# Kernel tuning notes

Measured on AMD Instinct MI355X. Metric: run time of the kernel, lower is better.

Reference implementation:

```python
import jax, jax.numpy as jnp
import numpy as np

B, T, H = 2, 2048, 2048
QH, KH, D = 16, 8, 128
F = 8192
EPS = 1e-06
MASK_VALUE = -1e30


def _rms_norm(x, gamma, eps=EPS):
    rms = jnp.sqrt(jnp.mean(x.astype(jnp.float32) ** 2, axis=-1, keepdims=True) + eps)
    return (gamma * x / rms).astype(jnp.bfloat16)


def _rope(x, sin, cos):
    # x: [B,T,h,D]; sin/cos: [B,T,D//2]
    x1, x2 = x[..., : x.shape[-1] // 2], x[..., x.shape[-1] // 2:]
    s, c = sin[:, :, None, :], cos[:, :, None, :]
    return jnp.concatenate([x1 * c - x2 * s, x2 * c + x1 * s], axis=-1)


def _attention(q, k, v, q_idx, k_idx, q_pos, k_pos):
    # q: [B,QH,T,D]; k,v: [B,KH,T,D]. Online-softmax tiling in the original is
    # mathematically identical to a single stable softmax over the full causal row.
    orig = q.dtype
    q = q.astype(jnp.float32)
    k = k.astype(jnp.float32)
    v = v.astype(jnp.float32)
    rep = q.shape[1] // k.shape[1]
    k = jnp.repeat(k, rep, axis=1)
    v = jnp.repeat(v, rep, axis=1)
    scale = 1.0 / jnp.sqrt(jnp.asarray(q.shape[-1], jnp.float32))
    s = jnp.einsum('bhqd,bhkd->bhqk', q, k) * scale
    mask = (q_idx[:, None, :, None] & k_idx[:, None, None, :]) & (
        q_pos[:, None, :, None] >= k_pos[:, None, None, :])
    s = jnp.where(mask, s, MASK_VALUE)
    p = jax.nn.softmax(s, axis=-1)
    o = jnp.einsum('bhqk,bhkd->bhqd', p, v)
    return o.astype(orig)


def _block(x, sin, cos, token_mask, pre_gamma, wq, wk, wv, q_gamma, k_gamma, wo,
           post_gamma, wg, wu, wd):
    bf = jnp.bfloat16
    Bx, Tx = x.shape[0], x.shape[1]
    x_norm = _rms_norm(x, pre_gamma)                     # bf16
    q = (x_norm @ wq.astype(bf)).reshape(Bx, Tx, QH, D)
    k = (x_norm @ wk.astype(bf)).reshape(Bx, Tx, KH, D)
    v = (x_norm @ wv.astype(bf)).reshape(Bx, Tx, KH, D)
    q = _rope(_rms_norm(q, q_gamma), sin, cos)           # promotes to f32 (matches flax)
    k = _rope(_rms_norm(k, k_gamma), sin, cos)
    idx = token_mask != 0
    pos = jax.lax.broadcasted_iota(jnp.int32, token_mask.shape, 1)
    attn = _attention(q.swapaxes(1, 2), k.swapaxes(1, 2), v.swapaxes(1, 2),
                      idx, idx, pos, pos)
    attn = attn.swapaxes(1, 2).reshape(Bx, Tx, QH * D)
    x = x + attn.astype(bf) @ wo.astype(bf)
    x_norm = _rms_norm(x, post_gamma)
    g = jax.nn.silu(x_norm @ wg.astype(bf))
    y = g * (x_norm @ wu.astype(bf))
    x = x + y @ wd.astype(bf)
    return x, k, v


def setup_inputs() -> dict:
    key = jax.random.key(0)
    ks = jax.random.split(key, 8)

    def w(kk, shape):
        return jax.random.normal(kk, shape, jnp.float32) * 0.02

    x = jax.random.normal(ks[0], (B, T, H), jnp.float32)
    pos = jnp.arange(T, dtype=jnp.float32)
    inv_freq = 1.0 / (10000.0 ** (jnp.arange(D // 2, dtype=jnp.float32) / (D // 2)))
    ang = pos[:, None] * inv_freq[None, :]
    sin = jnp.broadcast_to(jnp.sin(ang)[None], (B, T, D // 2))
    cos = jnp.broadcast_to(jnp.cos(ang)[None], (B, T, D // 2))
    return {
        'x': x, 'sin': sin, 'cos': cos,
        'token_mask': jnp.ones((B, T), jnp.int32),
        'layer_id': 0,
        'pre_gamma': jnp.ones((H,), jnp.float32),
        'wq': w(ks[1], (H, QH * D)),
        'wk': w(ks[2], (H, KH * D)),
        'wv': w(ks[3], (H, KH * D)),
        'q_gamma': jnp.ones((D,), jnp.float32),
        'k_gamma': jnp.ones((D,), jnp.float32),
        'wo': w(ks[4], (QH * D, H)),
        'post_gamma': jnp.ones((H,), jnp.float32),
        'wg': w(ks[5], (H, F)),
        'wu': w(ks[6], (H, F)),
        'wd': w(ks[7], (F, H)),
    }


def reference(x, sin, cos, token_mask, layer_id, pre_gamma, wq, wk, wv, q_gamma,
              k_gamma, wo, post_gamma, wg, wu, wd):
    # cache=None path: layer_id is unused.
    return _block(x, sin, cos, token_mask, pre_gamma, wq, wk, wv, q_gamma,
                  k_gamma, wo, post_gamma, wg, wu, wd)
```

## Files before the change

kernel.cpp:

```cpp
#include <hip/hip_runtime.h>
#include <hip/hip_bf16.h>


#define Bc  2
#define Tc  2048
#define Hc  2048
#define QHc 16
#define KHc 8
#define Dc  128
#define Fc  8192
#define Mc  (Bc*Tc)
#define FCHUNK 2048
#define EPSc 1e-6f
#define MASKVAL (-1e30f)

typedef __bf16  bf16x8 __attribute__((ext_vector_type(8)));
typedef short   short8 __attribute__((ext_vector_type(8)));
typedef float   f32x4  __attribute__((ext_vector_type(4)));

__device__ __forceinline__ float waveReduceSum(float v) {
    for (int off = 32; off > 0; off >>= 1) v += __shfl_down(v, off, 64);
    return v;
}

__device__ __forceinline__ void load_lds_16(const __hip_bfloat16* g,
                                            __hip_bfloat16* l) {
    __builtin_amdgcn_global_load_lds(
        (const __attribute__((address_space(1))) void*)g,
        (__attribute__((address_space(3))) void*)l, 16, 0, 0);
}

__global__ __launch_bounds__(256) void rmsnorm_f32_kernel(
    const float* __restrict__ in, const float* __restrict__ gamma,
    __hip_bfloat16* __restrict__ out, int width)
{
    const int row = blockIdx.x;
    const float* r = in + (size_t)row * width;
    float ss = 0.f;
    for (int i = threadIdx.x; i < width; i += 256) { float v = r[i]; ss += v * v; }
    ss = waveReduceSum(ss);
    __shared__ float red[4];
    if ((threadIdx.x & 63) == 0) red[threadIdx.x >> 6] = ss;
    __syncthreads();
    const float tot = red[0] + red[1] + red[2] + red[3];
    const float inv = 1.0f / sqrtf(tot / (float)width + EPSc);
    __hip_bfloat16* o = out + (size_t)row * width;
    for (int i = threadIdx.x; i < width; i += 256)
        o[i] = __float2bfloat16(gamma[i] * r[i] * inv);
}

__global__ __launch_bounds__(128) void qknorm_rope_kernel(
    const __hip_bfloat16* in, const float* __restrict__ gamma,
    const float* __restrict__ sinp, const float* __restrict__ cosp,
    __hip_bfloat16* outB, float* outF, int heads)
{
    const int row = blockIdx.x;
    const int bt  = row / heads;
    const int d   = threadIdx.x;
    const float v = __bfloat162float(in[(size_t)row * Dc + d]);
    float ss = waveReduceSum(v * v);
    __shared__ float red[2];
    __shared__ float nrm[Dc];
    if ((d & 63) == 0) red[d >> 6] = ss;
    __syncthreads();
    const float rms = sqrtf((red[0] + red[1]) * (1.0f / (float)Dc) + EPSc);
    const float xn = __bfloat162float(__float2bfloat16(gamma[d] * v / rms));
    nrm[d] = xn;
    __syncthreads();
    float res;
    if (d < 64) {
        const float s = sinp[(size_t)bt * 64 + d];
        const float c = cosp[(size_t)bt * 64 + d];
        res = nrm[d] * c - nrm[d + 64] * s;
    } else {
        const float s = sinp[(size_t)bt * 64 + (d - 64)];
        const float c = cosp[(size_t)bt * 64 + (d - 64)];
        res = nrm[d] * c + nrm[d - 64] * s;
    }
    outB[(size_t)row * Dc + d] = __float2bfloat16(res);
    if (outF) outF[(size_t)row * Dc + d] = res;
}

__global__ __launch_bounds__(256) void convert_transpose_kernel(
    const float* __restrict__ W, __hip_bfloat16* __restrict__ Wt, int K, int N)
{
    __shared__ float tile[32][33];
    const int tx = threadIdx.x & 31;
    const int ty = threadIdx.x >> 5;
    const int n0 = blockIdx.x * 32;
    const int k0 = blockIdx.y * 32;
    for (int r = 0; r < 4; ++r) {
        const int k = ty + r * 8;
        tile[k][tx] = W[(size_t)(k0 + k) * N + n0 + tx];
    }
    __syncthreads();
    for (int r = 0; r < 4; ++r) {
        const int n = ty + r * 8;
        Wt[(size_t)(n0 + n) * K + k0 + tx] = __float2bfloat16(tile[tx][n]);
    }
}


__device__ __forceinline__ void stage_unitA256(
    const __hip_bfloat16* __restrict__ Ag, __hip_bfloat16* bufBase,
    int m0, int lda, int kk0, int h, int tid)
{
#pragma unroll
    for (int p = 0; p < 2; ++p) {
        const int ci = p * 512 + tid;
        const int rl = ci >> 3;
        const int cc = ci & 7;
        const int grow = m0 + ((rl >> 6) * 128) + h * 64 + (rl & 63);
        const int scc = cc ^ (rl & 7);
        load_lds_16(Ag + (size_t)grow * lda + kk0 + scc * 8,
                    bufBase + h * 8192 + ci * 8);
    }
}

__device__ __forceinline__ void stage_unitB256(
    const __hip_bfloat16* __restrict__ Bg, __hip_bfloat16* bufBase,
    int n0, int ldt, int kk0, int h, int tid)
{
#pragma unroll
    for (int p = 0; p < 2; ++p) {
        const int ci = p * 512 + tid;
        const int rl = ci >> 3;
        const int cc = ci & 7;
        const int grow = n0 + h * 128 + rl;
        const int scc = cc ^ (rl & 7);
        load_lds_16(Bg + (size_t)grow * ldt + kk0 + scc * 8,
                    bufBase + h * 8192 + ci * 8);
    }
}

__device__ __forceinline__ bf16x8 read_frag256(const __hip_bfloat16* buf,
                                               int r, int w)
{
    const int cc = w ^ (r & 7);
    return *reinterpret_cast<const bf16x8*>(buf + r * 64 + cc * 8);
}

template <int MODE>
__global__ __launch_bounds__(512, 2) void gemm256_kernel(
    const __hip_bfloat16* __restrict__ A, const __hip_bfloat16* __restrict__ Bt,
    __hip_bfloat16* outB, float* outF, const float* resid,
    const __hip_bfloat16* gmul, int M, int N, int K, int lda, int ldt, int ldc)
{
    __shared__ __hip_bfloat16 smem[65536];
    __hip_bfloat16* Ab0 = smem;
    __hip_bfloat16* Ab1 = smem + 16384;
    __hip_bfloat16* Bb0 = smem + 32768;
    __hip_bfloat16* Bb1 = smem + 49152;

    if constexpr (MODE == 2) {
        A  += (size_t)blockIdx.z * K;
        Bt += (size_t)blockIdx.z * K;
    }

    const int tid  = threadIdx.x;
    const int lane = tid & 63;
    const int wave = tid >> 6;
    const int l15  = lane & 15;
    const int quad = lane >> 4;
    const int wm   = wave >> 2;
    const int wn   = wave & 3;
    const int m0   = blockIdx.y * 256;
    const int n0   = blockIdx.x * 256;
    const int NTt  = K >> 6;

    f32x4 acc[8][4];
    const f32x4 zero = {0.f, 0.f, 0.f, 0.f};
#pragma unroll
    for (int i = 0; i < 8; ++i)
#pragma unroll
        for (int j = 0; j < 4; ++j) acc[i][j] = zero;

    stage_unitA256(A, Ab0, m0, lda, 0, 0, tid);
    stage_unitA256(A, Ab0, m0, lda, 0, 1, tid);
    stage_unitB256(Bt, Bb0, n0, ldt, 0, 0, tid);
    stage_unitB256(Bt, Bb0, n0, ldt, 0, 1, tid);
    if (NTt > 1) {
        stage_unitA256(A, Ab1, m0, lda, 64, 0, tid);
        stage_unitB256(Bt, Bb1, n0, ldt, 64, 0, tid);
        stage_unitB256(Bt, Bb1, n0, ldt, 64, 1, tid);
    }
    asm volatile("s_waitcnt vmcnt(0)" ::: "memory");
    asm volatile("s_barrier" ::: "memory");

    bf16x8 bfr[4][2];
    bf16x8 af[4];

#define GB_READ_B(BB)                                                         \
    _Pragma("unroll")                                                         \
    for (int nt = 0; nt < 4; ++nt) {                                          \
        bfr[nt][0] = read_frag256(BB, wn * 64 + nt * 16 + l15, quad);         \
        bfr[nt][1] = read_frag256(BB, wn * 64 + nt * 16 + l15, 4 + quad);     \
    }
#define GB_READ_A(AB, MG, KS)                                                 \
    _Pragma("unroll")                                                         \
    for (int mq = 0; mq < 4; ++mq)                                            \
        af[mq] = read_frag256(AB, (MG)*128 + wm * 64 + mq * 16 + l15,         \
                              (KS)*4 + quad);
#define GB_MFMA(MG, KS)                                                       \
    __builtin_amdgcn_s_setprio(1);                                            \
    _Pragma("unroll")                                                         \
    for (int nt = 0; nt < 4; ++nt)                                            \
    _Pragma("unroll")                                                         \
    for (int mq = 0; mq < 4; ++mq)                                            \
        acc[(MG)*4 + mq][nt] = __builtin_amdgcn_mfma_f32_16x16x32_bf16(       \
            af[mq], bfr[nt][KS], acc[(MG)*4 + mq][nt], 0, 0, 0);              \
    __builtin_amdgcn_s_setprio(0);
#define SBAR256 asm volatile("s_barrier" ::: "memory")
#define VMC6    asm volatile("s_waitcnt vmcnt(6)" ::: "memory")

    const int nIter = NTt >> 1;
    for (int it = 0; it < nIter; ++it) {
        const int t1 = 2 * it + 1, t2 = 2 * it + 2, t3 = 2 * it + 3;
        GB_READ_B(Bb0); GB_READ_A(Ab0, 0, 0);
        stage_unitA256(A, Ab1, m0, lda, t1 * 64, 1, tid);
        SBAR256; GB_MFMA(0, 0); SBAR256;
        GB_READ_A(Ab0, 0, 1);
        if (t2 < NTt) stage_unitB256(Bt, Bb0, n0, ldt, t2 * 64, 0, tid);
        SBAR256; GB_MFMA(0, 1); SBAR256;
        GB_READ_A(Ab0, 1, 0);
        if (t2 < NTt) stage_unitB256(Bt, Bb0, n0, ldt, t2 * 64, 1, tid);
        SBAR256; GB_MFMA(1, 0); SBAR256;
        GB_READ_A(Ab0, 1, 1);
        if (t2 < NTt) stage_unitA256(A, Ab0, m0, lda, t2 * 64, 0, tid);
        SBAR256; GB_MFMA(1, 1); VMC6; SBAR256;
        GB_READ_B(Bb1); GB_READ_A(Ab1, 0, 0);
        if (t2 < NTt) stage_unitA256(A, Ab0, m0, lda, t2 * 64, 1, tid);
        SBAR256; GB_MFMA(0, 0); SBAR256;
        GB_READ_A(Ab1, 0, 1);
        if (t3 < NTt) stage_unitB256(Bt, Bb1, n0, ldt, t3 * 64, 0, tid);
        SBAR256; GB_MFMA(0, 1); SBAR256;
        GB_READ_A(Ab1, 1, 0);
        if (t3 < NTt) stage_unitB256(Bt, Bb1, n0, ldt, t3 * 64, 1, tid);
        SBAR256; GB_MFMA(1, 0); SBAR256;
        GB_READ_A(Ab1, 1, 1);
        if (t3 < NTt) stage_unitA256(A, Ab1, m0, lda, t3 * 64, 0, tid);
        SBAR256; GB_MFMA(1, 1); VMC6; SBAR256;
    }

#undef GB_READ_B
#undef GB_READ_A
#undef GB_MFMA
#undef SBAR256
#undef VMC6

#pragma unroll
    for (int m = 0; m < 8; ++m) {
#pragma unroll
        for (int nt = 0; nt < 4; ++nt) {
            const f32x4 a  = acc[m][nt];
            const int col  = n0 + wn * 64 + nt * 16 + l15;
            const int rowb = m0 + wm * 128 + (m >> 2) * 64 + (m & 3) * 16 + quad * 4;
#pragma unroll
            for (int r = 0; r < 4; ++r) {
                const size_t idx = (size_t)(rowb + r) * ldc + col;
                const float val = a[r];
                if constexpr (MODE == 0) {
                    outB[idx] = __float2bfloat16(val);
                } else if constexpr (MODE == 1) {
                    outF[idx] = resid[idx] +
                                __bfloat162float(__float2bfloat16(val));
                } else if constexpr (MODE == 2) {
                    unsafeAtomicAdd(&outF[idx], val);
                } else if constexpr (MODE == 3) {
                    const float g = __bfloat162float(gmul[idx]);
                    const float sil = __bfloat162float(
                        __float2bfloat16(g / (1.f + __expf(-g))));
                    const float u = __bfloat162float(__float2bfloat16(val));
                    outB[idx] = __float2bfloat16(sil * u);
                } else if constexpr (MODE == 4) {
                    const __hip_bfloat16 b = __float2bfloat16(val);
                    outB[idx] = b;
                    outF[idx] = __bfloat162float(b);
                } else {
                    if (n0 < 2048) {
                        outB[(size_t)(rowb + r) * 2048 + col] =
                            __float2bfloat16(val);
                    } else if (n0 < 3072) {
                        outB[8388608 + (size_t)(rowb + r) * 1024 + (col - 2048)] =
                            __float2bfloat16(val);
                    } else {
                        const __hip_bfloat16 b = __float2bfloat16(val);
                        outB[12582912 + (size_t)(rowb + r) * 1024 + (col - 3072)] = b;
                        outF[(size_t)(rowb + r) * 1024 + (col - 3072)] =
                            __bfloat162float(b);
                    }
                }
            }
        }
    }
}

template <int MODE>
__global__ __launch_bounds__(256) void gemm_kernel(
    const __hip_bfloat16* __restrict__ A, const float* __restrict__ Bw,
    __hip_bfloat16* outB, float* outF, const float* resid,
    const __hip_bfloat16* gmul, int M, int N, int K, int ldb)
{
    __shared__ __hip_bfloat16 As[128][32];
    __shared__ __hip_bfloat16 Bs[128][40];

    const int tid  = threadIdx.x;
    const int lane = tid & 63;
    const int wave = tid >> 6;
    const int l15  = lane & 15;
    const int quad = lane >> 4;
    const int q8   = quad * 8;
    const int wm   = wave >> 1;
    const int wn   = wave & 1;
    const int m0   = blockIdx.y * 128;
    const int n0   = blockIdx.x * 128;

    f32x4 acc[4][4];
    const f32x4 zero = {0.f, 0.f, 0.f, 0.f};
#pragma unroll
    for (int i = 0; i < 4; ++i)
#pragma unroll
        for (int j = 0; j < 4; ++j) acc[i][j] = zero;

    const int nK = K >> 5;
    for (int kt = 0; kt < nK; ++kt) {
        const int k0 = kt << 5;
        __syncthreads();
#pragma unroll
        for (int vv = 0; vv < 2; ++vv) {
            const int vi  = vv * 256 + tid;
            const int row = vi >> 2;
            const int col = (vi & 3) * 8;
            *(short8*)(&As[row][col]) =
                *(const short8*)(A + (size_t)(m0 + row) * K + k0 + col);
        }
        {
            const int n  = tid & 127;
            const int kk = tid >> 7;
            const float* bp = Bw + (size_t)k0 * ldb + n0 + n;
#pragma unroll
            for (int p = 0; p < 16; ++p) {
                const int k = p * 2 + kk;
                Bs[n][k] = __float2bfloat16(bp[(size_t)k * ldb]);
            }
        }
        __syncthreads();
        bf16x8 af[4], bfv[4];
#pragma unroll
        for (int mt = 0; mt < 4; ++mt)
            af[mt] = *reinterpret_cast<const bf16x8*>(&As[wm * 64 + mt * 16 + l15][q8]);
#pragma unroll
        for (int nt = 0; nt < 4; ++nt)
            bfv[nt] = *reinterpret_cast<const bf16x8*>(&Bs[wn * 64 + nt * 16 + l15][q8]);
#pragma unroll
        for (int mt = 0; mt < 4; ++mt)
#pragma unroll
            for (int nt = 0; nt < 4; ++nt)
                acc[mt][nt] = __builtin_amdgcn_mfma_f32_16x16x32_bf16(
                    af[mt], bfv[nt], acc[mt][nt], 0, 0, 0);
    }

#pragma unroll
    for (int mt = 0; mt < 4; ++mt) {
#pragma unroll
        for (int nt = 0; nt < 4; ++nt) {
            const f32x4 a  = acc[mt][nt];
            const int col  = n0 + wn * 64 + nt * 16 + l15;
            const int rowb = m0 + wm * 64 + mt * 16 + quad * 4;
#pragma unroll
            for (int r = 0; r < 4; ++r) {
                const size_t idx = (size_t)(rowb + r) * N + col;
                const float val = a[r];
                if constexpr (MODE == 0) {
                    outB[idx] = __float2bfloat16(val);
                } else if constexpr (MODE == 1) {
                    outF[idx] = resid[idx] +
                                __bfloat162float(__float2bfloat16(val));
                } else if constexpr (MODE == 3) {
                    const float g = __bfloat162float(gmul[idx]);
                    const float sil = __bfloat162float(
                        __float2bfloat16(g / (1.f + __expf(-g))));
                    const float u = __bfloat162float(__float2bfloat16(val));
                    outB[idx] = __float2bfloat16(sil * u);
                } else {
                    const __hip_bfloat16 b = __float2bfloat16(val);
                    outB[idx] = b;
                    outF[idx] = __bfloat162float(b);
                }
            }
        }
    }
}

__global__ __launch_bounds__(256) void flash_attn_kernel(
    const __hip_bfloat16* q, const __hip_bfloat16* __restrict__ k,
    const __hip_bfloat16* __restrict__ v, const int* __restrict__ mask,
    __hip_bfloat16* out)
{
    __shared__ unsigned short Ks[64][136];
    __shared__ unsigned short Vs[128][72];
    __shared__ unsigned short Ps[4][16][72];
    __shared__ int msk[64];

    const int tid  = threadIdx.x;
    const int lane = tid & 63;
    const int wave = tid >> 6;
    const int l15  = lane & 15;
    const int quad = lane >> 4;
    const int bh   = blockIdx.y;
    const int b    = bh >> 4;
    const int h    = bh & 15;
    const int kh   = h >> 1;
    const float scale = 0.08838834764831845f;

    const int skv = tid >> 4;
    const int sd0 = (tid & 15) * 8;
    const int vkv = tid & 63;
    const int vg0 = (tid >> 6) * 4;

    for (int half = 0; half < 2; ++half) {
        const int qt = (half == 0) ? (31 - (int)blockIdx.x) : (int)blockIdx.x;
        const int q0 = qt * 64;

        bf16x8 qf[4];
        {
            const __hip_bfloat16* qp =
                q + (((size_t)(b * Tc + q0 + wave * 16 + l15)) * QHc + h) * Dc;
#pragma unroll
            for (int kk = 0; kk < 4; ++kk)
                qf[kk] = *(const bf16x8*)(qp + kk * 32 + quad * 8);
        }

        float mrow[4] = {MASKVAL, MASKVAL, MASKVAL, MASKVAL};
        float lrow[4] = {0.f, 0.f, 0.f, 0.f};
        f32x4 oacc[8];
#pragma unroll
        for (int i = 0; i < 8; ++i) oacc[i] = (f32x4){0.f, 0.f, 0.f, 0.f};

        bf16x8 kreg[4];
        short8 vreg[4];
        int mreg = 0;
#pragma unroll
        for (int i = 0; i < 4; ++i)
            kreg[i] = *(const bf16x8*)(
                k + (((size_t)(b * Tc + skv + i * 16)) * KHc + kh) * Dc + sd0);
#pragma unroll
        for (int g = 0; g < 4; ++g)
            vreg[g] = *(const short8*)(
                v + (((size_t)(b * Tc + vkv)) * KHc + kh) * Dc + (vg0 + g) * 8);
        if (tid < 64) mreg = mask[b * Tc + tid];

        const int ktmax = qt;
        for (int kt = 0; kt <= ktmax; ++kt) {
            const int kvbase = kt * 64;
            __syncthreads();
#pragma unroll
            for (int i = 0; i < 4; ++i)
                *(bf16x8*)(&Ks[skv + i * 16][sd0]) = kreg[i];
#pragma unroll
            for (int g = 0; g < 4; ++g) {
                const int d0 = (vg0 + g) * 8;
#pragma unroll
                for (int j = 0; j < 8; ++j)
                    Vs[d0 + j][vkv] = (unsigned short)vreg[g][j];
            }
            if (tid < 64) msk[tid] = mreg;
            __syncthreads();

            if (kt < ktmax) {
                const int nb = (kt + 1) * 64;
#pragma unroll
                for (int i = 0; i < 4; ++i)
                    kreg[i] = *(const bf16x8*)(
                        k + (((size_t)(b * Tc + nb + skv + i * 16)) * KHc + kh) * Dc + sd0);
#pragma unroll
                for (int g = 0; g < 4; ++g)
                    vreg[g] = *(const short8*)(
                        v + (((size_t)(b * Tc + nb + vkv)) * KHc + kh) * Dc + (vg0 + g) * 8);
                if (tid < 64) mreg = mask[b * Tc + nb + tid];
            }

            f32x4 sacc[4];
#pragma unroll
            for (int nt = 0; nt < 4; ++nt) sacc[nt] = (f32x4){0.f, 0.f, 0.f, 0.f};
            __builtin_amdgcn_s_setprio(1);
#pragma unroll
            for (int nt = 0; nt < 4; ++nt)
#pragma unroll
                for (int kk = 0; kk < 4; ++kk) {
                    const bf16x8 kf = *(const bf16x8*)(&Ks[nt * 16 + l15][kk * 32 + quad * 8]);
                    sacc[nt] = __builtin_amdgcn_mfma_f32_16x16x32_bf16(
                        qf[kk], kf, sacc[nt], 0, 0, 0);
                }
            __builtin_amdgcn_s_setprio(0);

            float tmax[4] = {MASKVAL, MASKVAL, MASKVAL, MASKVAL};
#pragma unroll
            for (int nt = 0; nt < 4; ++nt) {
                const int kvpos  = kvbase + nt * 16 + l15;
                const bool kvld  = (msk[nt * 16 + l15] != 0);
#pragma unroll
                for (int r = 0; r < 4; ++r) {
                    const int qr = q0 + wave * 16 + quad * 4 + r;
                    float s = sacc[nt][r] * scale;
                    s = (kvld && kvpos <= qr) ? s : MASKVAL;
                    sacc[nt][r] = s;
                    tmax[r] = fmaxf(tmax[r], s);
                }
            }
#pragma unroll
            for (int r = 0; r < 4; ++r)
                for (int off = 1; off < 16; off <<= 1)
                    tmax[r] = fmaxf(tmax[r], __shfl_xor(tmax[r], off, 64));

            float alpha[4];
#pragma unroll
            for (int r = 0; r < 4; ++r) {
                const float mnew = fmaxf(mrow[r], tmax[r]);
                alpha[r] = __expf(mrow[r] - mnew);
                mrow[r]  = mnew;
            }
            float tsum[4] = {0.f, 0.f, 0.f, 0.f};
#pragma unroll
            for (int nt = 0; nt < 4; ++nt)
#pragma unroll
                for (int r = 0; r < 4; ++r) {
                    const float p = __expf(sacc[nt][r] - mrow[r]);
                    sacc[nt][r] = p;
                    tsum[r] += p;
                }
#pragma unroll
            for (int r = 0; r < 4; ++r)
                for (int off = 1; off < 16; off <<= 1)
                    tsum[r] += __shfl_xor(tsum[r], off, 64);
#pragma unroll
            for (int r = 0; r < 4; ++r)
                lrow[r] = lrow[r] * alpha[r] + tsum[r];

#pragma unroll
            for (int nt = 0; nt < 4; ++nt)
#pragma unroll
                for (int r = 0; r < 4; ++r) {
                    const __hip_bfloat16 pb = __float2bfloat16(sacc[nt][r]);
                    Ps[wave][quad * 4 + r][nt * 16 + l15] =
                        *(const unsigned short*)&pb;
                }

#pragma unroll
            for (int ntd = 0; ntd < 8; ++ntd)
#pragma unroll
                for (int r = 0; r < 4; ++r) oacc[ntd][r] *= alpha[r];
            bf16x8 pa[2];
#pragma unroll
            for (int kk2 = 0; kk2 < 2; ++kk2)
                pa[kk2] = *(const bf16x8*)(&Ps[wave][l15][kk2 * 32 + quad * 8]);
            __builtin_amdgcn_s_setprio(1);
#pragma unroll
            for (int ntd = 0; ntd < 8; ++ntd)
#pragma unroll
                for (int kk2 = 0; kk2 < 2; ++kk2) {
                    const bf16x8 vf = *(const bf16x8*)(
                        &Vs[ntd * 16 + l15][kk2 * 32 + quad * 8]);
                    oacc[ntd] = __builtin_amdgcn_mfma_f32_16x16x32_bf16(
                        pa[kk2], vf, oacc[ntd], 0, 0, 0);
                }
            __builtin_amdgcn_s_setprio(0);
        }

#pragma unroll
        for (int ntd = 0; ntd < 8; ++ntd)
#pragma unroll
            for (int r = 0; r < 4; ++r) {
                const float li = lrow[r];
                const float o  = (li > 0.f) ? oacc[ntd][r] / li : 0.f;
                const int qr   = q0 + wave * 16 + quad * 4 + r;
                out[(((size_t)(b * Tc + qr)) * QHc + h) * Dc + ntd * 16 + l15] =
                    __float2bfloat16(o);
            }
    }
}

extern "C" void kernel_launch(void* const* d_in, const int* in_sizes, int n_in,
                              void* d_out, int out_size, void* d_ws, size_t ws_size,
                              hipStream_t stream) {
    const float* x          = (const float*)d_in[0];
    const float* sinp       = (const float*)d_in[1];
    const float* cosp       = (const float*)d_in[2];
    const int*   token_mask = (const int*)d_in[3];
    const float* pre_gamma  = (const float*)d_in[5];
    const float* wq         = (const float*)d_in[6];
    const float* wk         = (const float*)d_in[7];
    const float* wv         = (const float*)d_in[8];
    const float* q_gamma    = (const float*)d_in[9];
    const float* k_gamma    = (const float*)d_in[10];
    const float* wo         = (const float*)d_in[11];
    const float* post_gamma = (const float*)d_in[12];
    const float* wg         = (const float*)d_in[13];
    const float* wu         = (const float*)d_in[14];
    const float* wd         = (const float*)d_in[15];

    float* outx = (float*)d_out;
    float* outk = outx + (size_t)Bc * Tc * Hc;
    float* outv = outk + (size_t)Bc * Tc * KHc * Dc;

    const bool fast = (ws_size >= 176160768ull);

    if (fast) {
        char* w = (char*)d_ws;
        __hip_bfloat16* wq_t  = (__hip_bfloat16*)(w);
        __hip_bfloat16* wk_t  = (__hip_bfloat16*)(w + 8388608);
        __hip_bfloat16* wv_t  = (__hip_bfloat16*)(w + 12582912);
        __hip_bfloat16* wo_t  = (__hip_bfloat16*)(w + 16777216);
        __hip_bfloat16* wg_t  = (__hip_bfloat16*)(w + 25165824);
        __hip_bfloat16* wu_t  = (__hip_bfloat16*)(w + 58720256);
        __hip_bfloat16* wd_t  = (__hip_bfloat16*)(w + 92274688);
        __hip_bfloat16* xnorm = (__hip_bfloat16*)(w + 125829120);
        __hip_bfloat16* qbuf  = (__hip_bfloat16*)(w + 142606336);
        __hip_bfloat16* kbuf  = (__hip_bfloat16*)(w + 159383552);
        __hip_bfloat16* vbuf  = (__hip_bfloat16*)(w + 167772160);
        __hip_bfloat16* Gbig  = qbuf;

        convert_transpose_kernel<<<dim3(Hc/32, Hc/32), 256, 0, stream>>>(wq, wq_t, Hc, Hc);
        convert_transpose_kernel<<<dim3((KHc*Dc)/32, Hc/32), 256, 0, stream>>>(wk, wk_t, Hc, KHc*Dc);
        convert_transpose_kernel<<<dim3((KHc*Dc)/32, Hc/32), 256, 0, stream>>>(wv, wv_t, Hc, KHc*Dc);
        convert_transpose_kernel<<<dim3(Hc/32, Hc/32), 256, 0, stream>>>(wo, wo_t, Hc, Hc);
        convert_transpose_kernel<<<dim3(Fc/32, Hc/32), 256, 0, stream>>>(wg, wg_t, Hc, Fc);
        convert_transpose_kernel<<<dim3(Fc/32, Hc/32), 256, 0, stream>>>(wu, wu_t, Hc, Fc);
        convert_transpose_kernel<<<dim3(Hc/32, Fc/32), 256, 0, stream>>>(wd, wd_t, Fc, Hc);

        rmsnorm_f32_kernel<<<Mc, 256, 0, stream>>>(x, pre_gamma, xnorm, Hc);

        gemm256_kernel<5><<<dim3(4096/256, Mc/256), 512, 0, stream>>>(
            xnorm, wq_t, qbuf, outv, nullptr, nullptr, Mc, 4096, Hc, Hc, Hc, 0);

        qknorm_rope_kernel<<<Mc*QHc, 128, 0, stream>>>(
            qbuf, q_gamma, sinp, cosp, qbuf, nullptr, QHc);
        qknorm_rope_kernel<<<Mc*KHc, 128, 0, stream>>>(
            kbuf, k_gamma, sinp, cosp, kbuf, outk, KHc);

        flash_attn_kernel<<<dim3(Tc/128, Bc*QHc), 256, 0, stream>>>(
            qbuf, kbuf, vbuf, token_mask, qbuf);

        gemm256_kernel<1><<<dim3(Hc/256, Mc/256), 512, 0, stream>>>(
            qbuf, wo_t, nullptr, outx, x, nullptr, Mc, Hc, Hc, Hc, Hc, Hc);

        rmsnorm_f32_kernel<<<Mc, 256, 0, stream>>>(outx, post_gamma, xnorm, Hc);

        for (int hh = 0; hh < 2; ++hh) {
            const __hip_bfloat16* wg_h = wg_t + (size_t)hh * 4096 * Hc;
            const __hip_bfloat16* wu_h = wu_t + (size_t)hh * 4096 * Hc;
            const __hip_bfloat16* wd_h = wd_t + (size_t)hh * 4096;
            gemm256_kernel<0><<<dim3(4096/256, Mc/256), 512, 0, stream>>>(
                xnorm, wg_h, Gbig, nullptr, nullptr, nullptr,
                Mc, 4096, Hc, Hc, Hc, 4096);
            gemm256_kernel<3><<<dim3(4096/256, Mc/256), 512, 0, stream>>>(
                xnorm, wu_h, Gbig, nullptr, nullptr, Gbig,
                Mc, 4096, Hc, Hc, Hc, 4096);
            gemm256_kernel<2><<<dim3(Hc/256, Mc/256, 2), 512, 0, stream>>>(
                Gbig, wd_h, nullptr, outx, nullptr, nullptr,
                Mc, Hc, 2048, 4096, Fc, Hc);
        }
    } else {
        char* w = (char*)d_ws;
        __hip_bfloat16* xnorm = (__hip_bfloat16*)(w);
        __hip_bfloat16* qbuf  = (__hip_bfloat16*)(w + 16777216);
        __hip_bfloat16* kbuf  = (__hip_bfloat16*)(w + 33554432);
        __hip_bfloat16* vbuf  = (__hip_bfloat16*)(w + 41943040);
        __hip_bfloat16* Gtmp  = qbuf;

        rmsnorm_f32_kernel<<<Mc, 256, 0, stream>>>(x, pre_gamma, xnorm, Hc);
        gemm_kernel<0><<<dim3(Hc/128, Mc/128), 256, 0, stream>>>(
            xnorm, wq, qbuf, nullptr, nullptr, nullptr, Mc, Hc, Hc, Hc);
        gemm_kernel<0><<<dim3((KHc*Dc)/128, Mc/128), 256, 0, stream>>>(
            xnorm, wk, kbuf, nullptr, nullptr, nullptr, Mc, KHc*Dc, Hc, KHc*Dc);
        gemm_kernel<4><<<dim3((KHc*Dc)/128, Mc/128), 256, 0, stream>>>(
            xnorm, wv, vbuf, outv, nullptr, nullptr, Mc, KHc*Dc, Hc, KHc*Dc);
        qknorm_rope_kernel<<<Mc*QHc, 128, 0, stream>>>(
            qbuf, q_gamma, sinp, cosp, qbuf, nullptr, QHc);
        qknorm_rope_kernel<<<Mc*KHc, 128, 0, stream>>>(
            kbuf, k_gamma, sinp, cosp, kbuf, outk, KHc);
        flash_attn_kernel<<<dim3(Tc/128, Bc*QHc), 256, 0, stream>>>(
            qbuf, kbuf, vbuf, token_mask, qbuf);
        gemm_kernel<1><<<dim3(Hc/128, Mc/128), 256, 0, stream>>>(
            qbuf, wo, nullptr, outx, x, nullptr, Mc, Hc, Hc, Hc);
        rmsnorm_f32_kernel<<<Mc, 256, 0, stream>>>(outx, post_gamma, xnorm, Hc);
        for (int c = 0; c < 4; ++c) {
            const float* wg_c = wg + (size_t)c * FCHUNK;
            const float* wu_c = wu + (size_t)c * FCHUNK;
            const float* wd_c = wd + (size_t)c * FCHUNK * Hc;
            gemm_kernel<0><<<dim3(FCHUNK/128, Mc/128), 256, 0, stream>>>(
                xnorm, wg_c, Gtmp, nullptr, nullptr, nullptr, Mc, FCHUNK, Hc, Fc);
            gemm_kernel<3><<<dim3(FCHUNK/128, Mc/128), 256, 0, stream>>>(
                xnorm, wu_c, Gtmp, nullptr, nullptr, Gtmp, Mc, FCHUNK, Hc, Fc);
            gemm_kernel<1><<<dim3(Hc/128, Mc/128), 256, 0, stream>>>(
                Gtmp, wd_c, nullptr, outx, outx, nullptr, Mc, Hc, FCHUNK, Hc);
        }
    }
}
```

Measured before the change: 1.165 ms.

## Pre-transpose V for attention, swizzle GEMM block order, batch weight conversions

Adds a bf16 transpose of V into a [KH*D, M] buffer so the attention kernel loads V rows with vector reads and writes them to LDS with 16-byte stores, replacing the scalar per-element transposed LDS writes. GEMM workgroup indices are remapped with a stride-8 swizzle so that consecutively scheduled blocks are spread across the tile grid, which may change cache locality. Weight convert-transpose launches are merged in pairs using blockIdx.z to cut launch count. The V transpose costs an extra pass over V and reuses the wk_t buffer as scratch, which is only safe if wk_t is no longer needed at that point.

```diff
diff --git a/kernel.cpp b/kernel.cpp
--- a/kernel.cpp
+++ b/kernel.cpp
@@ -81,9 +81,13 @@
     if (outF) outF[(size_t)row * Dc + d] = res;
 }
 
-__global__ __launch_bounds__(256) void convert_transpose_kernel(
-    const float* __restrict__ W, __hip_bfloat16* __restrict__ Wt, int K, int N)
-{
+__global__ __launch_bounds__(256) void convert_transpose2_kernel(
+    const float* __restrict__ W0, __hip_bfloat16* __restrict__ Wt0,
+    const float* __restrict__ W1, __hip_bfloat16* __restrict__ Wt1,
+    int K, int N)
+{
+    const float* W = blockIdx.z ? W1 : W0;
+    __hip_bfloat16* Wt = blockIdx.z ? Wt1 : Wt0;
     __shared__ float tile[32][33];
     const int tx = threadIdx.x & 31;
     const int ty = threadIdx.x >> 5;
@@ -100,6 +104,22 @@
     }
 }
 
+__global__ __launch_bounds__(256) void transpose_bf16_kernel(
+    const __hip_bfloat16* __restrict__ in, __hip_bfloat16* __restrict__ out,
+    int R, int C)
+{
+    __shared__ __hip_bfloat16 tile[32][33];
+    const int tx = threadIdx.x & 31;
+    const int ty = threadIdx.x >> 5;
+    const int c0 = blockIdx.x * 32;
+    const int r0 = blockIdx.y * 32;
+    for (int i = 0; i < 4; ++i)
+        tile[ty + i * 8][tx] = in[(size_t)(r0 + ty + i * 8) * C + c0 + tx];
+    __syncthreads();
+    for (int i = 0; i < 4; ++i)
+        out[(size_t)(c0 + ty + i * 8) * R + r0 + tx] = tile[tx][ty + i * 8];
+}
+
 
 __device__ __forceinline__ void stage_unitA256(
     const __hip_bfloat16* __restrict__ Ag, __hip_bfloat16* bufBase,
@@ -157,6 +177,12 @@
         Bt += (size_t)blockIdx.z * K;
     }
 
+    const int nwg  = gridDim.x * gridDim.y;
+    const int orig = blockIdx.y * gridDim.x + blockIdx.x;
+    const int swz  = (orig & 7) * (nwg >> 3) + (orig >> 3);
+    const int bxs  = swz % gridDim.x;
+    const int bys  = swz / gridDim.x;
+
     const int tid  = threadIdx.x;
     const int lane = tid & 63;
     const int wave = tid >> 6;
@@ -164,8 +190,8 @@
     const int quad = lane >> 4;
     const int wm   = wave >> 2;
     const int wn   = wave & 3;
-    const int m0   = blockIdx.y * 256;
-    const int n0   = blockIdx.x * 256;
+    const int m0   = bys * 256;
+    const int n0   = bxs * 256;
     const int NTt  = K >> 6;
 
     f32x4 acc[8][4];
@@ -392,6 +418,7 @@
     }
 }
 
+template <int VT>
 __global__ __launch_bounds__(256) void flash_attn_kernel(
     const __hip_bfloat16* q, const __hip_bfloat16* __restrict__ k,
     const __hip_bfloat16* __restrict__ v, const int* __restrict__ mask,
@@ -417,6 +444,9 @@
     const int sd0 = (tid & 15) * 8;
     const int vkv = tid & 63;
     const int vg0 = (tid >> 6) * 4;
+    const int vd  = tid >> 1;
+    const int vh  = (tid & 1) * 32;
+    const __hip_bfloat16* vtrow = v + (size_t)(kh * Dc + vd) * Mc + b * Tc;
 
     for (int half = 0; half < 2; ++half) {
         const int qt = (half == 0) ? (31 - (int)blockIdx.x) : (int)blockIdx.x;
@@ -438,16 +468,23 @@
         for (int i = 0; i < 8; ++i) oacc[i] = (f32x4){0.f, 0.f, 0.f, 0.f};
 
         bf16x8 kreg[4];
-        short8 vreg[4];
+        bf16x8 vregT[4];
+        short8 vregS[4];
         int mreg = 0;
 #pragma unroll
         for (int i = 0; i < 4; ++i)
             kreg[i] = *(const bf16x8*)(
                 k + (((size_t)(b * Tc + skv + i * 16)) * KHc + kh) * Dc + sd0);
-#pragma unroll
-        for (int g = 0; g < 4; ++g)
-            vreg[g] = *(const short8*)(
-                v + (((size_t)(b * Tc + vkv)) * KHc + kh) * Dc + (vg0 + g) * 8);
+        if constexpr (VT) {
+#pragma unroll
+            for (int j = 0; j < 4; ++j)
+                vregT[j] = *(const bf16x8*)(vtrow + vh + j * 8);
+        } else {
+#pragma unroll
+            for (int g = 0; g < 4; ++g)
+                vregS[g] = *(const short8*)(
+                    v + (((size_t)(b * Tc + vkv)) * KHc + kh) * Dc + (vg0 + g) * 8);
+        }
         if (tid < 64) mreg = mask[b * Tc + tid];
 
         const int ktmax = qt;
@@ -457,12 +494,18 @@
 #pragma unroll
             for (int i = 0; i < 4; ++i)
                 *(bf16x8*)(&Ks[skv + i * 16][sd0]) = kreg[i];
-#pragma unroll
-            for (int g = 0; g < 4; ++g) {
-                const int d0 = (vg0 + g) * 8;
-#pragma unroll
-                for (int j = 0; j < 8; ++j)
-                    Vs[d0 + j][vkv] = (unsigned short)vreg[g][j];
+            if constexpr (VT) {
+#pragma unroll
+                for (int j = 0; j < 4; ++j)
+                    *(bf16x8*)(&Vs[vd][vh + j * 8]) = vregT[j];
+            } else {
+#pragma unroll
+                for (int g = 0; g < 4; ++g) {
+                    const int d0 = (vg0 + g) * 8;
+#pragma unroll
+                    for (int j = 0; j < 8; ++j)
+                        Vs[d0 + j][vkv] = (unsigned short)vregS[g][j];
+                }
             }
             if (tid < 64) msk[tid] = mreg;
             __syncthreads();
@@ -473,10 +516,16 @@
                 for (int i = 0; i < 4; ++i)
                     kreg[i] = *(const bf16x8*)(
                         k + (((size_t)(b * Tc + nb + skv + i * 16)) * KHc + kh) * Dc + sd0);
-#pragma unroll
-                for (int g = 0; g < 4; ++g)
-                    vreg[g] = *(const short8*)(
-                        v + (((size_t)(b * Tc + nb + vkv)) * KHc + kh) * Dc + (vg0 + g) * 8);
+                if constexpr (VT) {
+#pragma unroll
+                    for (int j = 0; j < 4; ++j)
+                        vregT[j] = *(const bf16x8*)(vtrow + nb + vh + j * 8);
+                } else {
+#pragma unroll
+                    for (int g = 0; g < 4; ++g)
+                        vregS[g] = *(const short8*)(
+                            v + (((size_t)(b * Tc + nb + vkv)) * KHc + kh) * Dc + (vg0 + g) * 8);
+                }
                 if (tid < 64) mreg = mask[b * Tc + nb + tid];
             }
 
@@ -618,28 +667,33 @@
         __hip_bfloat16* qbuf  = (__hip_bfloat16*)(w + 142606336);
         __hip_bfloat16* kbuf  = (__hip_bfloat16*)(w + 159383552);
         __hip_bfloat16* vbuf  = (__hip_bfloat16*)(w + 167772160);
+        __hip_bfloat16* vtbuf = wk_t;
         __hip_bfloat16* Gbig  = qbuf;
 
-        convert_transpose_kernel<<<dim3(Hc/32, Hc/32), 256, 0, stream>>>(wq, wq_t, Hc, Hc);
-        convert_transpose_kernel<<<dim3((KHc*Dc)/32, Hc/32), 256, 0, stream>>>(wk, wk_t, Hc, KHc*Dc);
-        convert_transpose_kernel<<<dim3((KHc*Dc)/32, Hc/32), 256, 0, stream>>>(wv, wv_t, Hc, KHc*Dc);
-        convert_transpose_kernel<<<dim3(Hc/32, Hc/32), 256, 0, stream>>>(wo, wo_t, Hc, Hc);
-        convert_transpose_kernel<<<dim3(Fc/32, Hc/32), 256, 0, stream>>>(wg, wg_t, Hc, Fc);
-        convert_transpose_kernel<<<dim3(Fc/32, Hc/32), 256, 0, stream>>>(wu, wu_t, Hc, Fc);
-        convert_transpose_kernel<<<dim3(Hc/32, Fc/32), 256, 0, stream>>>(wd, wd_t, Fc, Hc);
+        convert_transpose2_kernel<<<dim3(Hc/32, Hc/32, 2), 256, 0, stream>>>(
+            wq, wq_t, wo, wo_t, Hc, Hc);
+        convert_transpose2_kernel<<<dim3((KHc*Dc)/32, Hc/32, 2), 256, 0, stream>>>(
+            wk, wk_t, wv, wv_t, Hc, KHc*Dc);
+        convert_transpose2_kernel<<<dim3(Fc/32, Hc/32, 2), 256, 0, stream>>>(
+            wg, wg_t, wu, wu_t, Hc, Fc);
+        convert_transpose2_kernel<<<dim3(Hc/32, Fc/32, 1), 256, 0, stream>>>(
+            wd, wd_t, wd, wd_t, Fc, Hc);
 
         rmsnorm_f32_kernel<<<Mc, 256, 0, stream>>>(x, pre_gamma, xnorm, Hc);
 
         gemm256_kernel<5><<<dim3(4096/256, Mc/256), 512, 0, stream>>>(
             xnorm, wq_t, qbuf, outv, nullptr, nullptr, Mc, 4096, Hc, Hc, Hc, 0);
+
+        transpose_bf16_kernel<<<dim3((KHc*Dc)/32, Mc/32), 256, 0, stream>>>(
+            vbuf, vtbuf, Mc, KHc*Dc);
 
         qknorm_rope_kernel<<<Mc*QHc, 128, 0, stream>>>(
             qbuf, q_gamma, sinp, cosp, qbuf, nullptr, QHc);
         qknorm_rope_kernel<<<Mc*KHc, 128, 0, stream>>>(
             kbuf, k_gamma, sinp, cosp, kbuf, outk, KHc);
 
-        flash_attn_kernel<<<dim3(Tc/128, Bc*QHc), 256, 0, stream>>>(
-            qbuf, kbuf, vbuf, token_mask, qbuf);
+        flash_attn_kernel<1><<<dim3(Tc/128, Bc*QHc), 256, 0, stream>>>(
+            qbuf, kbuf, vtbuf, token_mask, qbuf);
 
         gemm256_kernel<1><<<dim3(Hc/256, Mc/256), 512, 0, stream>>>(
             qbuf, wo_t, nullptr, outx, x, nullptr, Mc, Hc, Hc, Hc, Hc, Hc);
@@ -679,7 +733,7 @@
             qbuf, q_gamma, sinp, cosp, qbuf, nullptr, QHc);
         qknorm_rope_kernel<<<Mc*KHc, 128, 0, stream>>>(
             kbuf, k_gamma, sinp, cosp, kbuf, outk, KHc);
-        flash_attn_kernel<<<dim3(Tc/128, Bc*QHc), 256, 0, stream>>>(
+        flash_attn_kernel<0><<<dim3(Tc/128, Bc*QHc), 256, 0, stream>>>(
             qbuf, kbuf, vbuf, token_mask, qbuf);
         gemm_kernel<1><<<dim3(Hc/128, Mc/128), 256, 0, stream>>>(
             qbuf, wo, nullptr, outx, x, nullptr, Mc, Hc, Hc, Hc);
```

After: 1.128 ms. -3.2%, faster.
